# Kernel tuning notes

Measured on AMD Instinct MI355X. Metric: run time of the kernel, lower is better.

The kernel has to match this reference:

```python
import jax, jax.numpy as jnp
import numpy as np

D = 1024
N = 50000
SCALE = 1.0 / D  # scale torch.rand-style params to keep exp() in range


def _attention_module(X, W_alpha, a_alpha, b_alpha, W_sum):
    # a_w, b_w: [1, D] row vectors (a_alpha.T @ W_alpha)
    a_w = a_alpha[:, 0] @ W_alpha  # [D]
    b_w = b_alpha[:, 0] @ W_alpha  # [D]
    # score_j = a_w . X[0] + b_w . X[j]  -> alpha_j = exp(score_j)
    scores = jnp.dot(a_w, X[0]) + X @ b_w  # [N]
    alpha = jnp.exp(scores)  # [N]
    # weighted sum over neighbors, normalized by total alpha
    sum_output = (alpha @ X) / jnp.sum(alpha)  # [D]
    return sum_output @ W_sum  # [D]


def setup_inputs() -> dict:
    key = jax.random.key(0)
    ks = jax.random.split(key, 12)
    rand = lambda k, shape: jax.random.uniform(k, shape, dtype=jnp.float32) * SCALE
    return {
        "X_in": jax.random.normal(ks[0], (N, D), dtype=jnp.float32),
        "X_out": jax.random.normal(ks[1], (N, D), dtype=jnp.float32),
        "W_alpha_in": rand(ks[2], (D, D)),
        "a_alpha_in": rand(ks[3], (D, 1)),
        "b_alpha_in": rand(ks[4], (D, 1)),
        "W_sum_in": rand(ks[5], (D, D)),
        "W_alpha_out": rand(ks[6], (D, D)),
        "a_alpha_out": rand(ks[7], (D, 1)),
        "b_alpha_out": rand(ks[8], (D, 1)),
        "W_sum_out": rand(ks[9], (D, D)),
        "lin_W": jax.random.normal(ks[10], (D, 2 * D), dtype=jnp.float32) / np.sqrt(2 * D),
        "lin_b": jnp.zeros((D,), dtype=jnp.float32),
    }


def reference(X_in, X_out, W_alpha_in, a_alpha_in, b_alpha_in, W_sum_in,
              W_alpha_out, a_alpha_out, b_alpha_out, W_sum_out, lin_W, lin_b):
    res_in = _attention_module(X_in, W_alpha_in, a_alpha_in, b_alpha_in, W_sum_in)    # [D]
    res_out = _attention_module(X_out, W_alpha_out, a_alpha_out, b_alpha_out, W_sum_out)  # [D]
    attn = jnp.concatenate([res_in, res_out], axis=0)  # [2D]
    return jax.nn.elu(attn @ lin_W.T + lin_b)  # [D]
```

## Files before the change

kernel.cpp:

```cpp
#include <hip/hip_runtime.h>
#include <math.h>


#define DD 1024
#define NROWS 50000
#define GB 512
#define RB 4
#define NPART 16

__global__ __launch_bounds__(256) void vecmat_partial(
    const float* __restrict__ v0, const float* __restrict__ M0,
    const float* __restrict__ v1, const float* __restrict__ M1,
    float* __restrict__ out) {
  int bid = blockIdx.x;
  int module = bid >> 7;
  int r = bid & 127;
  int jb = r & 3;
  int ic = r >> 2;
  const float* __restrict__ v = module ? v1 : v0;
  const float* __restrict__ M = module ? M1 : M0;
  int j = jb * 256 + threadIdx.x;
  int i0 = ic * 32;
  float acc = 0.f;
#pragma unroll 8
  for (int i = i0; i < i0 + 32; ++i)
    acc = fmaf(v[i], M[i * DD + j], acc);
  atomicAdd(&out[module * DD + j], acc);
}

__global__ __launch_bounds__(256, 4) void attn_pass(
    const float* __restrict__ X0, const float* __restrict__ X1,
    const float* __restrict__ bw_all,
    float* __restrict__ num_part,
    float* __restrict__ den_part) {
  int bid = blockIdx.x;
  int module = (bid >= GB) ? 1 : 0;
  int b = module ? bid - GB : bid;
  const float* __restrict__ X = module ? X1 : X0;
  const float* __restrict__ bw = bw_all + module * DD;

  int tid = threadIdx.x;
  int lane = tid & 63;
  int wave = tid >> 6;
  int w = b * 4 + wave;
  const int WPM = GB * 4;

  float4 bwv[4], acc[4];
#pragma unroll
  for (int q = 0; q < 4; ++q) {
    bwv[q] = *reinterpret_cast<const float4*>(&bw[q * 256 + lane * 4]);
    acc[q] = make_float4(0.f, 0.f, 0.f, 0.f);
  }
  float asum = 0.f;

  for (int j0 = w * RB; j0 < NROWS; j0 += WPM * RB) {
    float4 xv[RB][4];
#pragma unroll
    for (int r = 0; r < RB; ++r) {
      const float4* __restrict__ row =
          reinterpret_cast<const float4*>(X + (size_t)(j0 + r) * DD);
#pragma unroll
      for (int q = 0; q < 4; ++q) xv[r][q] = row[q * 64 + lane];
    }
    float s[RB];
#pragma unroll
    for (int r = 0; r < RB; ++r) {
      float t = 0.f;
#pragma unroll
      for (int q = 0; q < 4; ++q) {
        t = fmaf(xv[r][q].x, bwv[q].x, t);
        t = fmaf(xv[r][q].y, bwv[q].y, t);
        t = fmaf(xv[r][q].z, bwv[q].z, t);
        t = fmaf(xv[r][q].w, bwv[q].w, t);
      }
      s[r] = t;
    }
#pragma unroll
    for (int off = 32; off >= 1; off >>= 1) {
#pragma unroll
      for (int r = 0; r < RB; ++r) s[r] += __shfl_xor(s[r], off, 64);
    }
#pragma unroll
    for (int r = 0; r < RB; ++r) {
      float alpha = __expf(s[r]);
      asum += alpha;
#pragma unroll
      for (int q = 0; q < 4; ++q) {
        acc[q].x = fmaf(alpha, xv[r][q].x, acc[q].x);
        acc[q].y = fmaf(alpha, xv[r][q].y, acc[q].y);
        acc[q].z = fmaf(alpha, xv[r][q].z, acc[q].z);
        acc[q].w = fmaf(alpha, xv[r][q].w, acc[q].w);
      }
    }
  }

  __shared__ float sdata[4][DD];
  __shared__ float dsum[4];
#pragma unroll
  for (int q = 0; q < 4; ++q)
    *reinterpret_cast<float4*>(&sdata[wave][q * 256 + lane * 4]) = acc[q];
  if (lane == 0) dsum[wave] = asum;
  __syncthreads();

  float4 a0 = *reinterpret_cast<float4*>(&sdata[0][tid * 4]);
  float4 a1 = *reinterpret_cast<float4*>(&sdata[1][tid * 4]);
  float4 a2 = *reinterpret_cast<float4*>(&sdata[2][tid * 4]);
  float4 a3 = *reinterpret_cast<float4*>(&sdata[3][tid * 4]);
  int p = module * NPART + (b & (NPART - 1));
  float* __restrict__ np = num_part + (size_t)p * DD;
  int c = tid * 4;
  atomicAdd(&np[c + 0], a0.x + a1.x + a2.x + a3.x);
  atomicAdd(&np[c + 1], a0.y + a1.y + a2.y + a3.y);
  atomicAdd(&np[c + 2], a0.z + a1.z + a2.z + a3.z);
  atomicAdd(&np[c + 3], a0.w + a1.w + a2.w + a3.w);
  if (tid == 0) atomicAdd(&den_part[p], dsum[0] + dsum[1] + dsum[2] + dsum[3]);
}

__global__ __launch_bounds__(256) void reduce_partials(
    const float* __restrict__ num_part, const float* __restrict__ den_part,
    float* __restrict__ num, float* __restrict__ den) {
  int idx = blockIdx.x * 256 + threadIdx.x;
  int m = idx >> 10;
  int i = idx & (DD - 1);
  float s = 0.f;
#pragma unroll
  for (int p = 0; p < NPART; ++p)
    s += num_part[((size_t)(m * NPART + p)) * DD + i];
  num[idx] = s;
  if (idx < 2) {
    float d = 0.f;
#pragma unroll
    for (int p = 0; p < NPART; ++p) d += den_part[idx * NPART + p];
    den[idx] = d;
  }
}

__global__ __launch_bounds__(256) void final_kernel(
    const float* __restrict__ res_raw, const float* __restrict__ den,
    const float* __restrict__ linW, const float* __restrict__ linb,
    float* __restrict__ out) {
  int k = blockIdx.x;
  int tid = threadIdx.x;
  float inv0 = 1.f / den[0];
  float inv1 = 1.f / den[1];
  const float* __restrict__ row = linW + (size_t)k * (2 * DD);
  float acc = 0.f;
#pragma unroll
  for (int s = 0; s < 8; ++s) {
    int m = s * 256 + tid;
    float attn = res_raw[m] * (m < DD ? inv0 : inv1);
    acc = fmaf(attn, row[m], acc);
  }
#pragma unroll
  for (int off = 32; off >= 1; off >>= 1) acc += __shfl_xor(acc, off, 64);
  __shared__ float wsum[4];
  int lane = tid & 63, wave = tid >> 6;
  if (lane == 0) wsum[wave] = acc;
  __syncthreads();
  if (tid == 0) {
    float v = wsum[0] + wsum[1] + wsum[2] + wsum[3] + linb[k];
    out[k] = v > 0.f ? v : expm1f(v);
  }
}

extern "C" void kernel_launch(void* const* d_in, const int* in_sizes, int n_in,
                              void* d_out, int out_size, void* d_ws, size_t ws_size,
                              hipStream_t stream) {
  const float* X_in    = (const float*)d_in[0];
  const float* X_out   = (const float*)d_in[1];
  const float* W_a_in  = (const float*)d_in[2];
  const float* b_a_in  = (const float*)d_in[4];
  const float* W_s_in  = (const float*)d_in[5];
  const float* W_a_out = (const float*)d_in[6];
  const float* b_a_out = (const float*)d_in[8];
  const float* W_s_out = (const float*)d_in[9];
  const float* linW    = (const float*)d_in[10];
  const float* linb    = (const float*)d_in[11];
  float* out = (float*)d_out;
  float* ws  = (float*)d_ws;

  float* bw       = ws;
  float* num_part = ws + 2048;
  float* den_part = ws + 34816;
  float* num      = ws + 34848;
  float* den      = ws + 36896;
  float* res_raw  = ws + 36898;

  hipMemsetAsync(d_ws, 0, 38946 * sizeof(float), stream);
  vecmat_partial<<<256, 256, 0, stream>>>(b_a_in, W_a_in, b_a_out, W_a_out, bw);
  attn_pass<<<2 * GB, 256, 0, stream>>>(X_in, X_out, bw, num_part, den_part);
  reduce_partials<<<8, 256, 0, stream>>>(num_part, den_part, num, den);
  vecmat_partial<<<256, 256, 0, stream>>>(num, W_s_in, num + 1024, W_s_out, res_raw);
  final_kernel<<<DD, 256, 0, stream>>>(res_raw, den, linW, linb, out);
}
```

Baseline: 444.8 us.

## Stream X rows through double-buffered LDS with async global-to-LDS loads

The main attention pass now stages each row into a per-wave double buffer in LDS using the global_load_lds builtin, prefetching two rows ahead with manual vmcnt waits. Each wave processes one row per iteration instead of batching four rows into registers. The aim is to keep memory requests in flight while cutting register pressure. It also drops the occupancy hint from launch bounds. The trade-offs are a larger LDS footprint of 32KB per block, which may limit resident blocks, plus extra LDS read traffic and hand-tuned waitcnt logic that could be fragile.

```diff
diff --git a/kernel.cpp b/kernel.cpp
--- a/kernel.cpp
+++ b/kernel.cpp
@@ -5,8 +5,12 @@
 #define DD 1024
 #define NROWS 50000
 #define GB 512
-#define RB 4
 #define NPART 16
+
+#define GLOAD_LDS16(g, l)                                    \
+  __builtin_amdgcn_global_load_lds(                          \
+      (const __attribute__((address_space(1))) void*)(g),    \
+      (__attribute__((address_space(3))) void*)(l), 16, 0, 0)
 
 __global__ __launch_bounds__(256) void vecmat_partial(
     const float* __restrict__ v0, const float* __restrict__ M0,
@@ -28,11 +32,14 @@
   atomicAdd(&out[module * DD + j], acc);
 }
 
-__global__ __launch_bounds__(256, 4) void attn_pass(
+__global__ __launch_bounds__(256) void attn_pass(
     const float* __restrict__ X0, const float* __restrict__ X1,
     const float* __restrict__ bw_all,
     float* __restrict__ num_part,
     float* __restrict__ den_part) {
+  __shared__ float lds[4 * 2 * DD];
+  __shared__ float dsum[4];
+
   int bid = blockIdx.x;
   int module = (bid >= GB) ? 1 : 0;
   int b = module ? bid - GB : bid;
@@ -43,7 +50,9 @@
   int lane = tid & 63;
   int wave = tid >> 6;
   int w = b * 4 + wave;
-  const int WPM = GB * 4;
+  const int W = GB * 4;
+
+  float* __restrict__ slot = &lds[wave * 2 * DD];
 
   float4 bwv[4], acc[4];
 #pragma unroll
@@ -53,59 +62,66 @@
   }
   float asum = 0.f;
 
-  for (int j0 = w * RB; j0 < NROWS; j0 += WPM * RB) {
-    float4 xv[RB][4];
-#pragma unroll
-    for (int r = 0; r < RB; ++r) {
-      const float4* __restrict__ row =
-          reinterpret_cast<const float4*>(X + (size_t)(j0 + r) * DD);
-#pragma unroll
-      for (int q = 0; q < 4; ++q) xv[r][q] = row[q * 64 + lane];
+  int myrows = (NROWS - 1 - w) / W + 1;
+
+  auto stage = [&](int it) {
+    long row = (long)w + (long)it * W;
+    const float* __restrict__ src = (row < NROWS) ? X + row * DD : X;
+    float* dst = slot + (it & 1) * DD;
+#pragma unroll
+    for (int i = 0; i < 4; ++i)
+      GLOAD_LDS16(src + i * 256 + lane * 4, dst + i * 256);
+  };
+
+  stage(0);
+  stage(1);
+
+  for (int it = 0; it < myrows; ++it) {
+    asm volatile("s_waitcnt vmcnt(4)" ::: "memory");
+    const float* __restrict__ s = slot + (it & 1) * DD;
+    float4 xv[4];
+#pragma unroll
+    for (int q = 0; q < 4; ++q)
+      xv[q] = *reinterpret_cast<const float4*>(&s[q * 256 + lane * 4]);
+    asm volatile("s_waitcnt lgkmcnt(0)" ::: "memory");
+    __builtin_amdgcn_sched_barrier(0);
+    stage(it + 2);
+
+    float t = 0.f;
+#pragma unroll
+    for (int q = 0; q < 4; ++q) {
+      t = fmaf(xv[q].x, bwv[q].x, t);
+      t = fmaf(xv[q].y, bwv[q].y, t);
+      t = fmaf(xv[q].z, bwv[q].z, t);
+      t = fmaf(xv[q].w, bwv[q].w, t);
     }
-    float s[RB];
-#pragma unroll
-    for (int r = 0; r < RB; ++r) {
-      float t = 0.f;
-#pragma unroll
-      for (int q = 0; q < 4; ++q) {
-        t = fmaf(xv[r][q].x, bwv[q].x, t);
-        t = fmaf(xv[r][q].y, bwv[q].y, t);
-        t = fmaf(xv[r][q].z, bwv[q].z, t);
-        t = fmaf(xv[r][q].w, bwv[q].w, t);
-      }
-      s[r] = t;
+#pragma unroll
+    for (int off = 32; off >= 1; off >>= 1) t += __shfl_xor(t, off, 64);
+    float alpha = __expf(t);
+    asum += alpha;
+#pragma unroll
+    for (int q = 0; q < 4; ++q) {
+      acc[q].x = fmaf(alpha, xv[q].x, acc[q].x);
+      acc[q].y = fmaf(alpha, xv[q].y, acc[q].y);
+      acc[q].z = fmaf(alpha, xv[q].z, acc[q].z);
+      acc[q].w = fmaf(alpha, xv[q].w, acc[q].w);
     }
-#pragma unroll
-    for (int off = 32; off >= 1; off >>= 1) {
-#pragma unroll
-      for (int r = 0; r < RB; ++r) s[r] += __shfl_xor(s[r], off, 64);
-    }
-#pragma unroll
-    for (int r = 0; r < RB; ++r) {
-      float alpha = __expf(s[r]);
-      asum += alpha;
-#pragma unroll
-      for (int q = 0; q < 4; ++q) {
-        acc[q].x = fmaf(alpha, xv[r][q].x, acc[q].x);
-        acc[q].y = fmaf(alpha, xv[r][q].y, acc[q].y);
-        acc[q].z = fmaf(alpha, xv[r][q].z, acc[q].z);
-        acc[q].w = fmaf(alpha, xv[r][q].w, acc[q].w);
-      }
-    }
-  }
-
-  __shared__ float sdata[4][DD];
-  __shared__ float dsum[4];
+  }
+
+  asm volatile("s_waitcnt vmcnt(0)" ::: "memory");
+  __syncthreads();
+
+  float* sdata = lds;
 #pragma unroll
   for (int q = 0; q < 4; ++q)
-    *reinterpret_cast<float4*>(&sdata[wave][q * 256 + lane * 4]) = acc[q];
+    *reinterpret_cast<float4*>(&sdata[wave * DD + q * 256 + lane * 4]) = acc[q];
   if (lane == 0) dsum[wave] = asum;
   __syncthreads();
 
-  float4 a0 = *reinterpret_cast<float4*>(&sdata[0][tid * 4]);
-  float4 a1 = *reinterpret_cast<float4*>(&sdata[1][tid * 4]);
-  float4 a2 = *reinterpret_cast<float4*>(&sdata[2][tid * 4]);
-  float4 a3 = *reinterpret_cast<float4*>(&sdata[3][tid * 4]);
+  float4 a0 = *reinterpret_cast<float4*>(&sdata[0 * DD + tid * 4]);
+  float4 a1 = *reinterpret_cast<float4*>(&sdata[1 * DD + tid * 4]);
+  float4 a2 = *reinterpret_cast<float4*>(&sdata[2 * DD + tid * 4]);
+  float4 a3 = *reinterpret_cast<float4*>(&sdata[3 * DD + tid * 4]);
   int p = module * NPART + (b & (NPART - 1));
   float* __restrict__ np = num_part + (size_t)p * DD;
   int c = tid * 4;
```

New measurement: 458.3 us. 3.0% more time.
